# Performance work log

Measured on AMD Instinct MI355X. Metric: run time of the kernel, lower is better.

The kernel has to match this reference:

```python
import jax, jax.numpy as jnp
import numpy as np

SEQ, B, IN, H, L = 512, 64, 128, 256, 6
STDV = 1.0 / (H ** 0.5)


def setup_inputs() -> dict:
    key = jax.random.key(0)
    ks = jax.random.split(key, 7)
    return {
        "x": jax.random.normal(ks[0], (SEQ, B, IN), jnp.float32),
        "h0": jax.random.normal(ks[1], (L, B, H), jnp.float32),
        "w_ih0": jax.random.uniform(ks[2], (3 * H, IN), jnp.float32, -STDV, STDV),
        "w_ih_rest": jax.random.uniform(ks[3], (L - 1, 3 * H, H), jnp.float32, -STDV, STDV),
        "w_hh": jax.random.uniform(ks[4], (L, 3 * H, H), jnp.float32, -STDV, STDV),
        "b_ih": jax.random.uniform(ks[5], (L, 3 * H), jnp.float32, -STDV, STDV),
        "b_hh": jax.random.uniform(ks[6], (L, 3 * H), jnp.float32, -STDV, STDV),
    }


def _gru_layer(x, h0, w_ih, w_hh, b_ih, b_hh):
    # Precompute input-side gate projections for all timesteps: (S, B, 3H)
    xg = jnp.einsum("sbi,gi->sbg", x, w_ih) + b_ih

    def step(h, xg_t):
        hg = h @ w_hh.T + b_hh  # (B, 3H)
        xr, xz, xn = jnp.split(xg_t, 3, axis=-1)
        hr, hz, hn = jnp.split(hg, 3, axis=-1)
        r = jax.nn.sigmoid(xr + hr)
        z = jax.nn.sigmoid(xz + hz)
        n = jnp.tanh(xn + r * hn)
        h_new = (1.0 - z) * n + z * h
        return h_new, h_new

    h_n, ys = jax.lax.scan(step, h0, xg)
    return ys, h_n


def reference(x, h0, w_ih0, w_ih_rest, w_hh, b_ih, b_hh):
    cur = x
    h_finals = []
    for i in range(L):
        w_ih = w_ih0 if i == 0 else w_ih_rest[i - 1]
        cur, h_n = _gru_layer(cur, h0[i], w_ih, w_hh[i], b_ih[i], b_hh[i])
        h_finals.append(h_n)
    return cur, jnp.stack(h_finals, axis=0)
```

## Files before the change

### kernel.cpp

```cpp
#include <hip/hip_runtime.h>

#define SEQ 512
#define BB 64
#define IN_DIM 128
#define HH 256
#define NL 6
#define G3 768
#define CHUNK 8
#define NCH (SEQ/CHUNK)
#define FSTR 16

typedef short short8 __attribute__((ext_vector_type(8)));
typedef short short4v __attribute__((ext_vector_type(4)));
typedef float f32x4 __attribute__((ext_vector_type(4)));

#define FR_SH ((size_t)5*4*CHUNK*BB*HH)
#define XG_SH ((size_t)NL*2*CHUNK*4*G3*16)
#define FLAGS_OFF_B ((FR_SH + XG_SH)*2)
#define NFLAG_INTS (16 + (24 + 96)*FSTR)
#define XGI(L,CS,TS,GI) (((((size_t)(L)*2+(CS))*CHUNK+(TS))*4+(GI))*((size_t)G3*16))

__device__ __forceinline__ short f2bf(float f) {
    unsigned u = __builtin_bit_cast(unsigned, f);
    u += 0x7fffu + ((u >> 16) & 1u);
    return (short)(u >> 16);
}
__device__ __forceinline__ float b2f(short s) {
    unsigned u = ((unsigned)(unsigned short)s) << 16;
    return __builtin_bit_cast(float, u);
}
__device__ __forceinline__ float sigm(float v) { return __fdividef(1.f, 1.f + __expf(-v)); }
__device__ __forceinline__ float tanh_f(float v) { float e = __expf(2.f * v); return 1.f - __fdividef(2.f, e + 1.f); }

__device__ __forceinline__ short8 pack_row(const float* p) {
    float4 a = *(const float4*)p;
    float4 c = *(const float4*)(p + 4);
    short8 v;
    v[0] = f2bf(a.x); v[1] = f2bf(a.y); v[2] = f2bf(a.z); v[3] = f2bf(a.w);
    v[4] = f2bf(c.x); v[5] = f2bf(c.y); v[6] = f2bf(c.z); v[7] = f2bf(c.w);
    return v;
}

struct XgRegs { short4v r0, r1, z0, z1, n0, n1; };
__device__ __forceinline__ XgRegs ld_xg(const short* pR, const short* pZ, const short* pN) {
    XgRegs o;
    asm volatile(
        "global_load_dwordx2 %0, %6, off sc0\n\t"
        "global_load_dwordx2 %1, %6, off offset:512 sc0\n\t"
        "global_load_dwordx2 %2, %7, off sc0\n\t"
        "global_load_dwordx2 %3, %7, off offset:512 sc0\n\t"
        "global_load_dwordx2 %4, %8, off sc0\n\t"
        "global_load_dwordx2 %5, %8, off offset:512 sc0"
        : "=&v"(o.r0), "=&v"(o.r1), "=&v"(o.z0), "=&v"(o.z1), "=&v"(o.n0), "=&v"(o.n1)
        : "v"(pR), "v"(pZ), "v"(pN) : "memory");
    return o;
}

__global__ __launch_bounds__(512, 1) void gru_persist(
    const float* __restrict__ x, const float* __restrict__ h0,
    const float* __restrict__ w_ih0, const float* __restrict__ w_ih_rest,
    const float* __restrict__ w_hh, const float* __restrict__ b_ih,
    const float* __restrict__ b_hh, float* __restrict__ y,
    short* __restrict__ fring, short* __restrict__ xg, int* __restrict__ flags)
{
    extern __shared__ char smem[];
    const int tid = threadIdx.x;
    const unsigned long long ddl = __builtin_amdgcn_s_memrealtime() + 800000000ull;

    const int xcc = __builtin_amdgcn_s_getreg(20 | (31 << 11)) & 0xf;
    if (xcc >= NL) return;
    __shared__ int s_slot;
    if (tid == 0) s_slot = __hip_atomic_fetch_add(&flags[xcc], 1, __ATOMIC_RELAXED, __HIP_MEMORY_SCOPE_AGENT);
    __syncthreads();
    const int slot = s_slot;
    if (slot >= 20) return;

    const int l = xcc;
    const int lane = tid & 63;
    const int wave = tid >> 6;
    const int q = lane >> 4;
    const int jj = lane & 15;

    int* recF  = flags + 16;
    int* projF = flags + 16 + 24 * FSTR;

    if (slot < 4) {
        const int g = slot;
        char* sWn = smem;
        char* sHB = smem + 131072;

        const float* whh = w_hh + (size_t)l * G3 * HH;
        short8 Wreg[4][8];
        #pragma unroll
        for (int i = 0; i < 4; ++i) {
            int row = (i >> 1) * HH + 32 * wave + 16 * (i & 1) + jj;
            #pragma unroll
            for (int kt = 0; kt < 8; ++kt)
                Wreg[i][kt] = pack_row(whh + (size_t)row * HH + kt * 32 + q * 8);
        }
        #pragma unroll
        for (int i2 = 0; i2 < 2; ++i2) {
            int row = 512 + 32 * wave + 16 * i2 + jj;
            #pragma unroll
            for (int kt = 0; kt < 8; ++kt) {
                short8 v = pack_row(whh + (size_t)row * HH + kt * 32 + q * 8);
                *(short8*)(sWn + ((size_t)(wave * 2 + i2) * 8 + kt) * 1024 + lane * 16) = v;
            }
        }
        float bhr[2], bhz[2], bhn2[2];
        #pragma unroll
        for (int jt2 = 0; jt2 < 2; ++jt2) {
            int j = 32 * wave + 16 * jt2 + jj;
            bhr[jt2]  = b_hh[l * G3 + j];
            bhz[jt2]  = b_hh[l * G3 + 256 + j];
            bhn2[jt2] = b_hh[l * G3 + 512 + j];
        }
        float hcur[2][4];
        #pragma unroll
        for (int jt2 = 0; jt2 < 2; ++jt2) {
            int j = 32 * wave + 16 * jt2 + jj;
            #pragma unroll
            for (int r = 0; r < 4; ++r)
                hcur[jt2][r] = h0[((size_t)l * BB + 16 * g + 4 * q + r) * HH + j];
        }
        for (int i = tid; i < 16 * 256; i += 512) {
            int b = i >> 8, j = i & 255;
            short hb = f2bf(h0[((size_t)l * BB + 16 * g + b) * HH + j]);
            *(short*)(sHB + b * 512 + ((2 * j) ^ ((b & 7) << 4))) = hb;
        }
        __syncthreads();

        const int cb = tid >> 5;
        const int cj0 = (tid & 31) * 8;
        const int laneoff = (32 * wave + jj) * 16 + 4 * q;
        const size_t tsStride = (size_t)4 * G3 * 16;

        for (int c = 0; c < NCH; ++c) {
            if (wave == 0) {
                const int* pa = nullptr; int tgt = 0;
                if (lane < 8) { pa = &projF[(l * 16 + 2 * lane + (g >> 1)) * FSTR]; tgt = c + 1; }
                else if (lane < 16 && l < NL - 1) { pa = &projF[((l + 1) * 16 + 2 * (lane - 8) + (g >> 1)) * FSTR]; tgt = c - 3; }
                int it = 0;
                for (;;) {
                    bool ok = true;
                    if (pa) ok = __hip_atomic_load((int*)pa, __ATOMIC_RELAXED, __HIP_MEMORY_SCOPE_AGENT) >= tgt;
                    if (__ballot(ok) == ~0ull) break;
                    __builtin_amdgcn_s_sleep(1);
                    if (((++it) & 63) == 0 && __builtin_amdgcn_s_memrealtime() > ddl) break;
                }
            }
            __syncthreads();

            short* frc = (l < NL - 1) ? fring + ((size_t)(l * 4 + (c & 3)) * CHUNK) * BB * HH : nullptr;
            const short* xgbase = xg + XGI(l, c & 1, 0, g);

            XgRegs xcur = ld_xg(xgbase + laneoff, xgbase + 256 * 16 + laneoff, xgbase + 512 * 16 + laneoff);

            for (int ts = 0; ts < CHUNK; ++ts) {
                const int t = c * CHUNK + ts;
                const int cur = t & 1, nxt = cur ^ 1;

                f32x4 acc[6] = {};
                #pragma unroll
                for (int kt = 0; kt < 8; ++kt) {
                    short8 af = *(const short8*)(sHB + cur * 8192 + (lane & 15) * 512
                                 + ((kt * 64 + q * 16) ^ ((lane & 7) << 4)));
                    acc[0] = __builtin_amdgcn_mfma_f32_16x16x32_bf16(af, Wreg[0][kt], acc[0], 0, 0, 0);
                    acc[1] = __builtin_amdgcn_mfma_f32_16x16x32_bf16(af, Wreg[1][kt], acc[1], 0, 0, 0);
                    acc[2] = __builtin_amdgcn_mfma_f32_16x16x32_bf16(af, Wreg[2][kt], acc[2], 0, 0, 0);
                    acc[3] = __builtin_amdgcn_mfma_f32_16x16x32_bf16(af, Wreg[3][kt], acc[3], 0, 0, 0);
                    short8 w4 = *(const short8*)(sWn + ((size_t)(wave * 2 + 0) * 8 + kt) * 1024 + lane * 16);
                    short8 w5 = *(const short8*)(sWn + ((size_t)(wave * 2 + 1) * 8 + kt) * 1024 + lane * 16);
                    acc[4] = __builtin_amdgcn_mfma_f32_16x16x32_bf16(af, w4, acc[4], 0, 0, 0);
                    acc[5] = __builtin_amdgcn_mfma_f32_16x16x32_bf16(af, w5, acc[5], 0, 0, 0);
                }
                asm volatile("s_waitcnt vmcnt(0)" ::: "memory");
                __builtin_amdgcn_sched_barrier(0);
                XgRegs xuse = xcur;
                const int tn = (ts + 1 < CHUNK) ? ts + 1 : ts;
                const short* nb = xgbase + (size_t)tn * tsStride;
                xcur = ld_xg(nb + laneoff, nb + 256 * 16 + laneoff, nb + 512 * 16 + laneoff);

                #pragma unroll
                for (int jt2 = 0; jt2 < 2; ++jt2) {
                    int j = 32 * wave + 16 * jt2 + jj;
                    short4v xrv = jt2 ? xuse.r1 : xuse.r0;
                    short4v xzv = jt2 ? xuse.z1 : xuse.z0;
                    short4v xnv = jt2 ? xuse.n1 : xuse.n0;
                    #pragma unroll
                    for (int r = 0; r < 4; ++r) {
                        int b = 4 * q + r;
                        float rg = sigm(acc[jt2][r] + b2f(xrv[r]) + bhr[jt2]);
                        float zg = sigm(acc[2 + jt2][r] + b2f(xzv[r]) + bhz[jt2]);
                        float ng = tanh_f(b2f(xnv[r]) + rg * (acc[4 + jt2][r] + bhn2[jt2]));
                        float hn = ng + zg * (hcur[jt2][r] - ng);
                        hcur[jt2][r] = hn;
                        *(short*)(sHB + nxt * 8192 + b * 512 + ((2 * j) ^ ((b & 7) << 4))) = f2bf(hn);
                    }
                }
                __syncthreads();

                short8 hv = *(const short8*)(sHB + nxt * 8192 + cb * 512 + ((2 * cj0) ^ ((cb & 7) << 4)));
                if (l < NL - 1) {
                    *(short8*)(frc + ((size_t)ts * BB + 16 * g + cb) * HH + cj0) = hv;
                } else {
                    float4 f0, f1;
                    f0.x = b2f(hv[0]); f0.y = b2f(hv[1]); f0.z = b2f(hv[2]); f0.w = b2f(hv[3]);
                    f1.x = b2f(hv[4]); f1.y = b2f(hv[5]); f1.z = b2f(hv[6]); f1.w = b2f(hv[7]);
                    float* yd = y + ((size_t)t * BB + 16 * g + cb) * HH + cj0;
                    *(float4*)yd = f0;
                    *(float4*)(yd + 4) = f1;
                }
            }
            __syncthreads();
            if (tid == 0)
                __hip_atomic_store(&recF[(l * 4 + g) * FSTR], c + 1, __ATOMIC_RELEASE, __HIP_MEMORY_SCOPE_AGENT);
        }
        #pragma unroll
        for (int jt2 = 0; jt2 < 2; ++jt2) {
            int j = 32 * wave + 16 * jt2 + jj;
            #pragma unroll
            for (int r = 0; r < 4; ++r)
                y[(size_t)SEQ * BB * HH + (size_t)l * BB * HH + ((size_t)16 * g + 4 * q + r) * HH + j] = hcur[jt2][r];
        }
    } else {
        const int p = slot - 4;
        const int t_p = p >> 1;
        const int bh = p & 1;
        const int KIN = (l == 0) ? IN_DIM : HH;
        const int KTp = (l == 0) ? 4 : 8;
        char* sWp = smem;

        const float* wih = (l == 0) ? w_ih0 : (w_ih_rest + (size_t)(l - 1) * G3 * HH);
        short8 Wp[4][8];
        #pragma unroll
        for (int i = 0; i < 4; ++i) {
            int row = (6 * wave + i) * 16 + jj;
            for (int kt = 0; kt < KTp; ++kt)
                Wp[i][kt] = pack_row(wih + (size_t)row * KIN + kt * 32 + q * 8);
        }
        #pragma unroll
        for (int i2 = 0; i2 < 2; ++i2) {
            int row = (6 * wave + 4 + i2) * 16 + jj;
            for (int kt = 0; kt < KTp; ++kt) {
                short8 v = pack_row(wih + (size_t)row * KIN + kt * 32 + q * 8);
                *(short8*)(sWp + ((size_t)(wave * 2 + i2) * 8 + kt) * 1024 + lane * 16) = v;
            }
        }
        float bias[6];
        #pragma unroll
        for (int i = 0; i < 6; ++i)
            bias[i] = b_ih[l * G3 + (6 * wave + i) * 16 + jj];
        __syncthreads();

        for (int c = 0; c < NCH; ++c) {
            if (wave == 0) {
                const int* pa = nullptr; int tgt = 0;
                if (lane < 2) { if (l > 0) { pa = &recF[((l - 1) * 4 + 2 * bh + lane) * FSTR]; tgt = c + 1; } }
                else if (lane < 4) { pa = &recF[(l * 4 + 2 * bh + (lane - 2)) * FSTR]; tgt = c - 1; }
                int it = 0;
                for (;;) {
                    bool ok = true;
                    if (pa) ok = __hip_atomic_load((int*)pa, __ATOMIC_RELAXED, __HIP_MEMORY_SCOPE_AGENT) >= tgt;
                    if (__ballot(ok) == ~0ull) break;
                    __builtin_amdgcn_s_sleep(1);
                    if (((++it) & 63) == 0 && __builtin_amdgcn_s_memrealtime() > ddl) break;
                }
                if (l > 0) __builtin_amdgcn_fence(__ATOMIC_ACQUIRE, "agent");
            }
            __syncthreads();

            const short* frs = (l > 0)
                ? fring + ((size_t)((l - 1) * 4 + (c & 3)) * CHUNK + t_p) * BB * HH : nullptr;

            #pragma unroll
            for (int mt2 = 0; mt2 < 2; ++mt2) {
                const int bgl = 32 * bh + 16 * mt2 + (lane & 15);
                short8 afv[8];
                for (int kt = 0; kt < KTp; ++kt) {
                    if (l == 0)
                        afv[kt] = pack_row(x + ((size_t)(c * CHUNK + t_p) * BB + bgl) * IN_DIM + kt * 32 + q * 8);
                    else
                        afv[kt] = *(const short8*)(frs + (size_t)bgl * HH + kt * 32 + q * 8);
                }
                f32x4 acc[6] = {};
                for (int kt = 0; kt < KTp; ++kt) {
                    short8 af = afv[kt];
                    acc[0] = __builtin_amdgcn_mfma_f32_16x16x32_bf16(af, Wp[0][kt], acc[0], 0, 0, 0);
                    acc[1] = __builtin_amdgcn_mfma_f32_16x16x32_bf16(af, Wp[1][kt], acc[1], 0, 0, 0);
                    acc[2] = __builtin_amdgcn_mfma_f32_16x16x32_bf16(af, Wp[2][kt], acc[2], 0, 0, 0);
                    acc[3] = __builtin_amdgcn_mfma_f32_16x16x32_bf16(af, Wp[3][kt], acc[3], 0, 0, 0);
                    short8 w4 = *(const short8*)(sWp + ((size_t)(wave * 2 + 0) * 8 + kt) * 1024 + lane * 16);
                    short8 w5 = *(const short8*)(sWp + ((size_t)(wave * 2 + 1) * 8 + kt) * 1024 + lane * 16);
                    acc[4] = __builtin_amdgcn_mfma_f32_16x16x32_bf16(af, w4, acc[4], 0, 0, 0);
                    acc[5] = __builtin_amdgcn_mfma_f32_16x16x32_bf16(af, w5, acc[5], 0, 0, 0);
                }
                short* xgd = xg + XGI(l, c & 1, t_p, 2 * bh + mt2);
                #pragma unroll
                for (int i = 0; i < 6; ++i) {
                    int r = (6 * wave + i) * 16 + jj;
                    short4v o;
                    o[0] = f2bf(acc[i][0] + bias[i]);
                    o[1] = f2bf(acc[i][1] + bias[i]);
                    o[2] = f2bf(acc[i][2] + bias[i]);
                    o[3] = f2bf(acc[i][3] + bias[i]);
                    *(short4v*)(xgd + (size_t)r * 16 + 4 * q) = o;
                }
            }
            __syncthreads();
            if (tid == 0)
                __hip_atomic_store(&projF[(l * 16 + p) * FSTR], c + 1, __ATOMIC_RELEASE, __HIP_MEMORY_SCOPE_AGENT);
        }
    }
}

extern "C" void kernel_launch(void* const* d_in, const int* in_sizes, int n_in,
                              void* d_out, int out_size, void* d_ws, size_t ws_size,
                              hipStream_t stream) {
    (void)in_sizes; (void)n_in; (void)out_size; (void)ws_size;
    const float* x         = (const float*)d_in[0];
    const float* h0        = (const float*)d_in[1];
    const float* w_ih0     = (const float*)d_in[2];
    const float* w_ih_rest = (const float*)d_in[3];
    const float* w_hh      = (const float*)d_in[4];
    const float* b_ih      = (const float*)d_in[5];
    const float* b_hh      = (const float*)d_in[6];
    float* y = (float*)d_out;

    short* fring = (short*)d_ws;
    short* xgb   = fring + FR_SH;
    int*   flags = (int*)((char*)d_ws + FLAGS_OFF_B);

    (void)hipMemsetAsync(flags, 0, NFLAG_INTS * sizeof(int), stream);
    gru_persist<<<256, 512, 147456, stream>>>(
        x, h0, w_ih0, w_ih_rest, w_hh, b_ih, b_hh, y, fring, xgb, flags);
}
```

Baseline: 4.096 ms.

## Replace per-block flag polling with aggregated counters and XCD-leader acquire

Swaps the many per-block progress flags for per-layer atomic counters. Recurrent blocks bump a done counter and a leader publishes a single flag. Projection blocks increment shared done and consumed counters, and only projection block 0 does the agent-scope acquire fence, then signals the others through an xcdReady flag. Previous-layer activations are now read with sc0 inline-asm loads that bypass cached stale data, batching eight loads before one wait. The aim is fewer polled addresses and fences per chunk. The cost is extra serialization through the leader, and the weaker fetch-add/relaxed ordering risks memory-ordering bugs.

```diff
diff --git a/kernel.cpp b/kernel.cpp
--- a/kernel.cpp
+++ b/kernel.cpp
@@ -17,7 +17,7 @@
 #define FR_SH ((size_t)5*4*CHUNK*BB*HH)
 #define XG_SH ((size_t)NL*2*CHUNK*4*G3*16)
 #define FLAGS_OFF_B ((FR_SH + XG_SH)*2)
-#define NFLAG_INTS (16 + (24 + 96)*FSTR)
+#define NFLAG_INTS (16 + 5*NL*FSTR)
 #define XGI(L,CS,TS,GI) (((((size_t)(L)*2+(CS))*CHUNK+(TS))*4+(GI))*((size_t)G3*16))
 
 __device__ __forceinline__ short f2bf(float f) {
@@ -56,6 +56,25 @@
     return o;
 }
 
+struct Fr8 { short8 v0, v1, v2, v3, v4, v5, v6, v7; };
+__device__ __forceinline__ Fr8 ld_fr8_sc0(const char* p) {
+    Fr8 r;
+    asm volatile(
+        "global_load_dwordx4 %0, %8, off sc0\n\t"
+        "global_load_dwordx4 %1, %8, off offset:64 sc0\n\t"
+        "global_load_dwordx4 %2, %8, off offset:128 sc0\n\t"
+        "global_load_dwordx4 %3, %8, off offset:192 sc0\n\t"
+        "global_load_dwordx4 %4, %8, off offset:256 sc0\n\t"
+        "global_load_dwordx4 %5, %8, off offset:320 sc0\n\t"
+        "global_load_dwordx4 %6, %8, off offset:384 sc0\n\t"
+        "global_load_dwordx4 %7, %8, off offset:448 sc0\n\t"
+        "s_waitcnt vmcnt(0)"
+        : "=&v"(r.v0), "=&v"(r.v1), "=&v"(r.v2), "=&v"(r.v3),
+          "=&v"(r.v4), "=&v"(r.v5), "=&v"(r.v6), "=&v"(r.v7)
+        : "v"(p) : "memory");
+    return r;
+}
+
 __global__ __launch_bounds__(512, 1) void gru_persist(
     const float* __restrict__ x, const float* __restrict__ h0,
     const float* __restrict__ w_ih0, const float* __restrict__ w_ih_rest,
@@ -81,8 +100,11 @@
     const int q = lane >> 4;
     const int jj = lane & 15;
 
-    int* recF  = flags + 16;
-    int* projF = flags + 16 + 24 * FSTR;
+    int* recF     = flags + 16;
+    int* recDone  = flags + 16 + 1 * NL * FSTR;
+    int* projDone = flags + 16 + 2 * NL * FSTR;
+    int* consumed = flags + 16 + 3 * NL * FSTR;
+    int* xcdReady = flags + 16 + 4 * NL * FSTR;
 
     if (slot < 4) {
         const int g = slot;
@@ -138,8 +160,8 @@
         for (int c = 0; c < NCH; ++c) {
             if (wave == 0) {
                 const int* pa = nullptr; int tgt = 0;
-                if (lane < 8) { pa = &projF[(l * 16 + 2 * lane + (g >> 1)) * FSTR]; tgt = c + 1; }
-                else if (lane < 16 && l < NL - 1) { pa = &projF[((l + 1) * 16 + 2 * (lane - 8) + (g >> 1)) * FSTR]; tgt = c - 3; }
+                if (lane == 0) { pa = &projDone[l * FSTR]; tgt = 16 * (c + 1); }
+                else if (lane == 1 && l < NL - 1 && c >= 4) { pa = &consumed[(l + 1) * FSTR]; tgt = 16 * (c - 3); }
                 int it = 0;
                 for (;;) {
                     bool ok = true;
@@ -213,8 +235,18 @@
                 }
             }
             __syncthreads();
-            if (tid == 0)
-                __hip_atomic_store(&recF[(l * 4 + g) * FSTR], c + 1, __ATOMIC_RELEASE, __HIP_MEMORY_SCOPE_AGENT);
+
+            if (tid == 0) {
+                __hip_atomic_fetch_add(&recDone[l * FSTR], 1, __ATOMIC_RELAXED, __HIP_MEMORY_SCOPE_AGENT);
+                if (g == 0) {
+                    int it = 0;
+                    while (__hip_atomic_load(&recDone[l * FSTR], __ATOMIC_RELAXED, __HIP_MEMORY_SCOPE_AGENT) < 4 * (c + 1)) {
+                        __builtin_amdgcn_s_sleep(1);
+                        if (((++it) & 63) == 0 && __builtin_amdgcn_s_memrealtime() > ddl) break;
+                    }
+                    __hip_atomic_store(&recF[l * FSTR], c + 1, __ATOMIC_RELEASE, __HIP_MEMORY_SCOPE_AGENT);
+                }
+            }
         }
         #pragma unroll
         for (int jt2 = 0; jt2 < 2; ++jt2) {
@@ -256,8 +288,11 @@
         for (int c = 0; c < NCH; ++c) {
             if (wave == 0) {
                 const int* pa = nullptr; int tgt = 0;
-                if (lane < 2) { if (l > 0) { pa = &recF[((l - 1) * 4 + 2 * bh + lane) * FSTR]; tgt = c + 1; } }
-                else if (lane < 4) { pa = &recF[(l * 4 + 2 * bh + (lane - 2)) * FSTR]; tgt = c - 1; }
+                if (lane == 0) { pa = &recF[l * FSTR]; tgt = c - 1; }
+                else if (lane == 1 && l > 0) {
+                    if (p == 0) { pa = &recF[(l - 1) * FSTR]; tgt = c + 1; }
+                    else        { pa = &xcdReady[l * FSTR];   tgt = c + 1; }
+                }
                 int it = 0;
                 for (;;) {
                     bool ok = true;
@@ -266,7 +301,11 @@
                     __builtin_amdgcn_s_sleep(1);
                     if (((++it) & 63) == 0 && __builtin_amdgcn_s_memrealtime() > ddl) break;
                 }
-                if (l > 0) __builtin_amdgcn_fence(__ATOMIC_ACQUIRE, "agent");
+                if (l > 0 && p == 0) {
+                    __builtin_amdgcn_fence(__ATOMIC_ACQUIRE, "agent");
+                    if (lane == 0)
+                        __hip_atomic_store(&xcdReady[l * FSTR], c + 1, __ATOMIC_RELAXED, __HIP_MEMORY_SCOPE_AGENT);
+                }
             }
             __syncthreads();
 
@@ -277,11 +316,13 @@
             for (int mt2 = 0; mt2 < 2; ++mt2) {
                 const int bgl = 32 * bh + 16 * mt2 + (lane & 15);
                 short8 afv[8];
-                for (int kt = 0; kt < KTp; ++kt) {
-                    if (l == 0)
+                if (l == 0) {
+                    for (int kt = 0; kt < 4; ++kt)
                         afv[kt] = pack_row(x + ((size_t)(c * CHUNK + t_p) * BB + bgl) * IN_DIM + kt * 32 + q * 8);
-                    else
-                        afv[kt] = *(const short8*)(frs + (size_t)bgl * HH + kt * 32 + q * 8);
+                } else {
+                    Fr8 fr = ld_fr8_sc0((const char*)(frs + (size_t)bgl * HH + q * 8));
+                    afv[0] = fr.v0; afv[1] = fr.v1; afv[2] = fr.v2; afv[3] = fr.v3;
+                    afv[4] = fr.v4; afv[5] = fr.v5; afv[6] = fr.v6; afv[7] = fr.v7;
                 }
                 f32x4 acc[6] = {};
                 for (int kt = 0; kt < KTp; ++kt) {
@@ -308,8 +349,11 @@
                 }
             }
             __syncthreads();
-            if (tid == 0)
-                __hip_atomic_store(&projF[(l * 16 + p) * FSTR], c + 1, __ATOMIC_RELEASE, __HIP_MEMORY_SCOPE_AGENT);
+            if (tid == 0) {
+                __hip_atomic_fetch_add(&projDone[l * FSTR], 1, __ATOMIC_RELAXED, __HIP_MEMORY_SCOPE_AGENT);
+                if (l > 0)
+                    __hip_atomic_fetch_add(&consumed[l * FSTR], 1, __ATOMIC_RELAXED, __HIP_MEMORY_SCOPE_AGENT);
+            }
         }
     }
 }
```

Result: slower. 8.749 ms (+113.6%).

## Replace release/acquire fences with cache-bypassing stores and loads for ring buffer

Applied to the files above, without the earlier changes.

The recurrent workers now write their hidden-state ring with sc0 sc1 stores that bypass the caches. The projection workers read that ring with matching bypassing loads in one batched asm block. This lets the flag stores become relaxed and removes the agent-scope acquire fence, avoiding cache writeback and invalidate work on every chunk handoff in the latency-bound recurrence. The projF flag is also relaxed while the xg stores remain ordinary stores, so visibility and ordering of the projection outputs across XCCs is no longer guaranteed by a release.

```diff
diff --git a/kernel.cpp b/kernel.cpp
--- a/kernel.cpp
+++ b/kernel.cpp
@@ -39,6 +39,10 @@
     v[0] = f2bf(a.x); v[1] = f2bf(a.y); v[2] = f2bf(a.z); v[3] = f2bf(a.w);
     v[4] = f2bf(c.x); v[5] = f2bf(c.y); v[6] = f2bf(c.z); v[7] = f2bf(c.w);
     return v;
+}
+
+__device__ __forceinline__ void st16_ic(void* p, short8 v) {
+    asm volatile("global_store_dwordx4 %0, %1, off sc0 sc1" :: "v"(p), "v"(v) : "memory");
 }
 
 struct XgRegs { short4v r0, r1, z0, z1, n0, n1; };
@@ -54,6 +58,25 @@
         : "=&v"(o.r0), "=&v"(o.r1), "=&v"(o.z0), "=&v"(o.z1), "=&v"(o.n0), "=&v"(o.n1)
         : "v"(pR), "v"(pZ), "v"(pN) : "memory");
     return o;
+}
+
+struct Fr8 { short8 v0, v1, v2, v3, v4, v5, v6, v7; };
+__device__ __forceinline__ Fr8 ld_fr8_ic(const char* p) {
+    Fr8 r;
+    asm volatile(
+        "global_load_dwordx4 %0, %8, off sc0 sc1\n\t"
+        "global_load_dwordx4 %1, %8, off offset:64 sc0 sc1\n\t"
+        "global_load_dwordx4 %2, %8, off offset:128 sc0 sc1\n\t"
+        "global_load_dwordx4 %3, %8, off offset:192 sc0 sc1\n\t"
+        "global_load_dwordx4 %4, %8, off offset:256 sc0 sc1\n\t"
+        "global_load_dwordx4 %5, %8, off offset:320 sc0 sc1\n\t"
+        "global_load_dwordx4 %6, %8, off offset:384 sc0 sc1\n\t"
+        "global_load_dwordx4 %7, %8, off offset:448 sc0 sc1\n\t"
+        "s_waitcnt vmcnt(0)"
+        : "=&v"(r.v0), "=&v"(r.v1), "=&v"(r.v2), "=&v"(r.v3),
+          "=&v"(r.v4), "=&v"(r.v5), "=&v"(r.v6), "=&v"(r.v7)
+        : "v"(p) : "memory");
+    return r;
 }
 
 __global__ __launch_bounds__(512, 1) void gru_persist(
@@ -202,7 +225,7 @@
 
                 short8 hv = *(const short8*)(sHB + nxt * 8192 + cb * 512 + ((2 * cj0) ^ ((cb & 7) << 4)));
                 if (l < NL - 1) {
-                    *(short8*)(frc + ((size_t)ts * BB + 16 * g + cb) * HH + cj0) = hv;
+                    st16_ic(frc + ((size_t)ts * BB + 16 * g + cb) * HH + cj0, hv);
                 } else {
                     float4 f0, f1;
                     f0.x = b2f(hv[0]); f0.y = b2f(hv[1]); f0.z = b2f(hv[2]); f0.w = b2f(hv[3]);
@@ -214,7 +237,7 @@
             }
             __syncthreads();
             if (tid == 0)
-                __hip_atomic_store(&recF[(l * 4 + g) * FSTR], c + 1, __ATOMIC_RELEASE, __HIP_MEMORY_SCOPE_AGENT);
+                __hip_atomic_store(&recF[(l * 4 + g) * FSTR], c + 1, __ATOMIC_RELAXED, __HIP_MEMORY_SCOPE_AGENT);
         }
         #pragma unroll
         for (int jt2 = 0; jt2 < 2; ++jt2) {
@@ -266,7 +289,6 @@
                     __builtin_amdgcn_s_sleep(1);
                     if (((++it) & 63) == 0 && __builtin_amdgcn_s_memrealtime() > ddl) break;
                 }
-                if (l > 0) __builtin_amdgcn_fence(__ATOMIC_ACQUIRE, "agent");
             }
             __syncthreads();
 
@@ -277,11 +299,13 @@
             for (int mt2 = 0; mt2 < 2; ++mt2) {
                 const int bgl = 32 * bh + 16 * mt2 + (lane & 15);
                 short8 afv[8];
-                for (int kt = 0; kt < KTp; ++kt) {
-                    if (l == 0)
+                if (l == 0) {
+                    for (int kt = 0; kt < 4; ++kt)
                         afv[kt] = pack_row(x + ((size_t)(c * CHUNK + t_p) * BB + bgl) * IN_DIM + kt * 32 + q * 8);
-                    else
-                        afv[kt] = *(const short8*)(frs + (size_t)bgl * HH + kt * 32 + q * 8);
+                } else {
+                    Fr8 fr = ld_fr8_ic((const char*)(frs + (size_t)bgl * HH + q * 8));
+                    afv[0] = fr.v0; afv[1] = fr.v1; afv[2] = fr.v2; afv[3] = fr.v3;
+                    afv[4] = fr.v4; afv[5] = fr.v5; afv[6] = fr.v6; afv[7] = fr.v7;
                 }
                 f32x4 acc[6] = {};
                 for (int kt = 0; kt < KTp; ++kt) {
@@ -309,7 +333,7 @@
             }
             __syncthreads();
             if (tid == 0)
-                __hip_atomic_store(&projF[(l * 16 + p) * FSTR], c + 1, __ATOMIC_RELEASE, __HIP_MEMORY_SCOPE_AGENT);
+                __hip_atomic_store(&projF[(l * 16 + p) * FSTR], c + 1, __ATOMIC_RELAXED, __HIP_MEMORY_SCOPE_AGENT);
         }
     }
 }
```

Measured after the change: 8.725 ms. 113% more time.
